# Kernel tuning notes

Measured on AMD Instinct MI355X. Metric: run time of the kernel, lower is better.

Reference implementation:

```python
import jax, jax.numpy as jnp
import numpy as np

H = 1024   # hidden_dim
I = 256    # input_dim
T = 128    # time_step
NW = 4     # input_num (weeks)
N = 100    # stocks = 5 categories * 20
C, G = 5, 20


def gru(x, Wih, Whh, bih, bhh):
    """Torch-style single-layer GRU. x: (B,T,I) batch_first -> (B,T,H). Gate order r,z,n."""
    gx = jnp.einsum('bti,gi->btg', x, Wih) + bih  # (B,T,3H) input projections precomputed
    h0 = jnp.zeros((x.shape[0], Whh.shape[1]), x.dtype)

    def step(h, g):
        gh = h @ Whh.T + bhh
        xr, xz, xn = jnp.split(g, 3, axis=-1)
        hr, hz, hn = jnp.split(gh, 3, axis=-1)
        r = jax.nn.sigmoid(xr + hr)
        z = jax.nn.sigmoid(xz + hz)
        n = jnp.tanh(xn + r * hn)
        h = (1.0 - z) * n + z * h
        return h, h

    _, ys = jax.lax.scan(step, h0, jnp.swapaxes(gx, 0, 1))
    return jnp.swapaxes(ys, 0, 1)


def att_block(x, W, b):
    """AttentionBlock: x (B,T,D); Linear over time axis, softmax over time, weighted sum."""
    xt = jnp.swapaxes(x, 1, 2)                    # (B,D,T)
    probs = jax.nn.softmax(xt @ W.T + b, axis=-1) # (B,D,T)
    probs = jnp.swapaxes(probs, 1, 2)             # (B,T,D)
    return (probs * x).sum(axis=1)                # (B,D)


def gat(x, edges, W, a_s, a_d, bias):
    """PyG GATConv, heads=1, add_self_loops=True, leaky_relu slope 0.2."""
    n = x.shape[0]
    h = x @ W.T                                   # (n,H)
    loop = jnp.arange(n)
    src = jnp.concatenate([edges[0], loop])
    dst = jnp.concatenate([edges[1], loop])
    e = jax.nn.leaky_relu((h @ a_s)[src] + (h @ a_d)[dst], 0.2)
    m = jax.ops.segment_max(e, dst, num_segments=n)
    ex = jnp.exp(e - m[dst])
    s = jax.ops.segment_sum(ex, dst, num_segments=n)
    alpha = ex / s[dst]
    return jax.ops.segment_sum(alpha[:, None] * h[src], dst, num_segments=n) + bias


def setup_inputs() -> dict:
    key = jax.random.key(0)
    ks = iter(jax.random.split(key, 64))
    p = lambda *s: jax.random.normal(next(ks), s, dtype=jnp.float32) * 0.05
    inp = {}
    for i in range(NW):
        inp[f'w{i}'] = jax.random.normal(next(ks), (N, T, I), dtype=jnp.float32)
    inp['inner_edge'] = jax.random.randint(next(ks), (2, 2000), 0, N, dtype=jnp.int32)
    inp['outer_edge'] = jax.random.randint(next(ks), (2, 25), 0, C, dtype=jnp.int32)
    # per-week sequence encoders (stacked)
    inp['enc_Wih'] = p(NW, 3 * H, I); inp['enc_Whh'] = p(NW, 3 * H, H)
    inp['enc_bih'] = p(NW, 3 * H);    inp['enc_bhh'] = p(NW, 3 * H)
    inp['enc_attW'] = p(NW, T, T);    inp['enc_attb'] = p(NW, T)
    # weekly GRU (not batch_first in torch!)
    inp['wk_Wih'] = p(3 * H, H); inp['wk_Whh'] = p(3 * H, H)
    inp['wk_bih'] = p(3 * H);    inp['wk_bhh'] = p(3 * H)
    inp['wkatt_W'] = p(NW, NW); inp['wkatt_b'] = p(NW)
    inp['pool_W'] = p(G, G);    inp['pool_b'] = p(G)
    inp['ig_W'] = p(H, H); inp['ig_as'] = p(H); inp['ig_ad'] = p(H); inp['ig_b'] = p(H)
    inp['cg_W'] = p(H, H); inp['cg_as'] = p(H); inp['cg_ad'] = p(H); inp['cg_b'] = p(H)
    inp['fus_W'] = p(H, 3 * H); inp['fus_b'] = p(H)
    inp['reg_W'] = p(1, H); inp['reg_b'] = p(1)
    inp['cls_W'] = p(1, H); inp['cls_b'] = p(1)
    return inp


def reference(w0, w1, w2, w3, inner_edge, outer_edge,
              enc_Wih, enc_Whh, enc_bih, enc_bhh, enc_attW, enc_attb,
              wk_Wih, wk_Whh, wk_bih, wk_bhh, wkatt_W, wkatt_b,
              pool_W, pool_b, ig_W, ig_as, ig_ad, ig_b,
              cg_W, cg_as, cg_ad, cg_b, fus_W, fus_b,
              reg_W, reg_b, cls_W, cls_b):
    weeks = [w0, w1, w2, w3]
    embs = []
    for i in range(NW):
        seq = gru(weeks[i], enc_Wih[i], enc_Whh[i], enc_bih[i], enc_bhh[i])  # (N,T,H)
        embs.append(att_block(seq, enc_attW[i], enc_attb[i])[:, None, :])    # (N,1,H)
    we = jnp.concatenate(embs, axis=1)                                       # (N,NW,H)
    # torch nn.GRU default seq-major: scans over dim0 (N stocks), batch=NW
    we = jnp.swapaxes(gru(jnp.swapaxes(we, 0, 1), wk_Wih, wk_Whh, wk_bih, wk_bhh), 0, 1)
    wav = att_block(we, wkatt_W, wkatt_b)                                    # (N,H)
    inner = gat(wav, inner_edge, ig_W, ig_as, ig_ad, ig_b).reshape(C, G, -1)
    wav3 = wav.reshape(C, G, -1)
    cat = att_block(wav3, pool_W, pool_b)                                    # (C,H)
    cat = gat(cat, outer_edge, cg_W, cg_as, cg_ad, cg_b)                     # (C,H)
    cat = jnp.broadcast_to(cat[:, None, :], (C, G, cat.shape[-1]))
    f = jnp.concatenate([wav3, cat, inner], axis=-1)                         # (C,G,3H)
    f = jax.nn.relu(f @ fus_W.T + fus_b)
    reg = (f @ reg_W.T + reg_b).reshape(-1)
    cls = jax.nn.sigmoid(f @ cls_W.T + cls_b).reshape(-1)
    return reg, cls
```

## Files before the change

kernel.cpp:

```cpp
#include <hip/hip_runtime.h>
#include <hip/hip_bf16.h>

#define NW 4
#define NST 100
#define TT 128
#define II 256
#define HH 1024
#define H3 3072

typedef _Float16 h8 __attribute__((ext_vector_type(8)));
typedef float f4 __attribute__((ext_vector_type(4)));

__device__ __forceinline__ float sigf(float x) { return 1.0f / (1.0f + expf(-x)); }

__device__ __forceinline__ float4 ld_f4_sc1(const float* p) {
    union { unsigned long long u[2]; float4 v; } r;
    r.u[0] = __hip_atomic_load((unsigned long long*)p, __ATOMIC_RELAXED, __HIP_MEMORY_SCOPE_AGENT);
    r.u[1] = __hip_atomic_load((unsigned long long*)p + 1, __ATOMIC_RELAXED, __HIP_MEMORY_SCOPE_AGENT);
    return r.v;
}
__device__ __forceinline__ float ld_f_sc1(const float* p) {
    return __hip_atomic_load((float*)p, __ATOMIC_RELAXED, __HIP_MEMORY_SCOPE_AGENT);
}

__device__ __forceinline__ void spin_wait(unsigned* f, unsigned t) {
    int guard = 0;
    while (__hip_atomic_load(f, __ATOMIC_RELAXED, __HIP_MEMORY_SCOPE_AGENT) <= t) {
        __builtin_amdgcn_s_sleep(1);
        if (++guard > (1 << 21)) break;
    }
}

__global__ void zero_k(float* a, int n) {
    int i = blockIdx.x * 256 + threadIdx.x;
    if (i < n) a[i] = 0.0f;
}

__global__ void convW_k(const float* __restrict__ Whh, const float* __restrict__ Wih,
                        _Float16* __restrict__ Wc) {
    int col = blockIdx.x * 256 + threadIdx.x;
    int r = blockIdx.y;
    int w = blockIdx.z;
    float v = (col < HH) ? Whh[((size_t)w * H3 + r) * HH + col]
                         : Wih[((size_t)w * H3 + r) * II + (col - HH)];
    Wc[((size_t)w * H3 + r) * 1280 + col] = (_Float16)v;
}

__global__ void convWk_k(const float* __restrict__ src, _Float16* __restrict__ dst) {
    int col = blockIdx.x * 256 + threadIdx.x;
    int r = blockIdx.y;
    dst[(size_t)r * HH + col] = (_Float16)src[(size_t)r * HH + col];
}

__global__ void xcvt_k(const float* __restrict__ x0, const float* __restrict__ x1,
                       const float* __restrict__ x2, const float* __restrict__ x3,
                       _Float16* __restrict__ xT) {
    int idx = blockIdx.x * 256 + threadIdx.x;
    int k8 = idx & 31;
    int m  = (idx >> 5) & 127;
    int t  = (idx >> 12) & 127;
    int w  = idx >> 19;
    const float* xw = (w == 0) ? x0 : (w == 1) ? x1 : (w == 2) ? x2 : x3;
    h8 hv = {};
    if (m < NST) {
        const float* s = xw + ((size_t)m * TT + t) * II + k8 * 8;
        float4 fa = *(const float4*)s;
        float4 fb = *(const float4*)(s + 4);
        hv[0] = (_Float16)fa.x; hv[1] = (_Float16)fa.y;
        hv[2] = (_Float16)fa.z; hv[3] = (_Float16)fa.w;
        hv[4] = (_Float16)fb.x; hv[5] = (_Float16)fb.y;
        hv[6] = (_Float16)fb.z; hv[7] = (_Float16)fb.w;
    }
    *(h8*)&xT[(((size_t)w * TT + t) * 128 + m) * II + k8 * 8] = hv;
}

__global__ void wTcvt_k(const float* __restrict__ attW, float* __restrict__ wT) {
    int tp = threadIdx.x;
    int t  = blockIdx.x;
    int w  = blockIdx.y;
    wT[((size_t)w * TT + t) * TT + tp] = attW[((size_t)w * TT + tp) * TT + t];
}

__global__ void convB_k(const float* __restrict__ bih, const float* __restrict__ bhh,
                        float* __restrict__ bc) {
    int j = blockIdx.x * 256 + threadIdx.x;
    int w = blockIdx.y;
    const float* bi = bih + w * H3;
    const float* bh = bhh + w * H3;
    float* o = bc + w * 4096;
    o[j] = bi[j] + bh[j];
    o[1024 + j] = bi[1024 + j] + bh[1024 + j];
    o[2048 + j] = bi[2048 + j];
    o[3072 + j] = bh[2048 + j];
}

#define ENC_LDS_HALFS (40 * 3 * 16 * 32)
#define ENC_LDS_BYTES (ENC_LDS_HALFS * 2)

__global__ __launch_bounds__(256) void enc_fused_k(
    const _Float16* __restrict__ Wc, const float* __restrict__ bc,
    const _Float16* __restrict__ xT,
    _Float16* __restrict__ hhA, _Float16* __restrict__ hhB,
    _Float16* __restrict__ seq, unsigned* flags)
{
    extern __shared__ _Float16 Bs[];

    int id = blockIdx.x;
    int rr = id & 7, qq = id >> 3;
    int w  = rr >> 1;
    int bx = qq * 2 + (rr & 1);
    int j0 = bx * 16;

    const _Float16* Wcw = Wc + (size_t)w * H3 * 1280;
    const float* bcw = bc + w * 4096;
    _Float16* hA = hhA + (size_t)w * 128 * HH;
    _Float16* hB = hhB + (size_t)w * 128 * HH;
    unsigned* fw = flags + (size_t)w * 64 * 16;

    int tid = threadIdx.x;
    int lane = tid & 63, wi = tid >> 6, quad = lane >> 4, l15 = lane & 15;

    if (tid < 192) {
        int brow = tid >> 2, bseg = tid & 3;
        int g = brow >> 4, jj = brow & 15;
        const _Float16* bsrc =
            Wcw + (size_t)(g * 1024 + j0 + jj) * 1280 + bseg * 8;
        #pragma unroll 8
        for (int c = 0; c < 40; c++) {
            uint4 v = *(const uint4*)(bsrc + c * 32);
            *(uint4*)&Bs[(((size_t)c * 3 + g) * 16 + jj) * 32 + bseg * 8] = v;
        }
    }
    __syncthreads();

    int j = j0 + l15;
    float br = bcw[j], bz = bcw[1024 + j], bni = bcw[2048 + j], bnh = bcw[3072 + j];
    int r0 = wi * 32 + l15, r1 = wi * 32 + 16 + l15;
    float hreg[2][4] = {};

    for (int t = 0; t < TT; t++) {
        const _Float16* hin = (t & 1) ? hB : hA;
        _Float16* hout = (t & 1) ? hA : hB;
        const _Float16* xt = xT + ((size_t)w * TT + t) * 128 * II;
        const _Float16* pA0h = hin + (size_t)r0 * HH + quad * 8;
        const _Float16* pA1h = hin + (size_t)r1 * HH + quad * 8;
        const _Float16* pA0x = xt + (size_t)r0 * II + quad * 8;
        const _Float16* pA1x = xt + (size_t)r1 * II + quad * 8;

        f4 aR[2] = {}, aZ[2] = {}, aNH[2] = {}, aNX[2] = {};

        h8 rb0[8], rb1[8];
        #pragma unroll
        for (int u = 0; u < 8; u++) {
            rb0[u] = *(const h8*)(pA0h + u * 32);
            rb1[u] = *(const h8*)(pA1h + u * 32);
        }

        #pragma unroll 8
        for (int c = 0; c < 40; c++) {
            int u = c & 7;
            h8 a0 = rb0[u], a1 = rb1[u];
            int cn = c + 8;
            if (cn < 32) {
                rb0[u] = *(const h8*)(pA0h + cn * 32);
                rb1[u] = *(const h8*)(pA1h + cn * 32);
            } else if (cn < 40) {
                rb0[u] = *(const h8*)(pA0x + (cn - 32) * 32);
                rb1[u] = *(const h8*)(pA1x + (cn - 32) * 32);
            }
            const _Float16* bb = &Bs[(size_t)c * 1536];
            h8 bf0 = *(const h8*)&bb[l15 * 32 + quad * 8];
            h8 bf1 = *(const h8*)&bb[512 + l15 * 32 + quad * 8];
            h8 bf2 = *(const h8*)&bb[1024 + l15 * 32 + quad * 8];
            aR[0] = __builtin_amdgcn_mfma_f32_16x16x32_f16(a0, bf0, aR[0], 0, 0, 0);
            aR[1] = __builtin_amdgcn_mfma_f32_16x16x32_f16(a1, bf0, aR[1], 0, 0, 0);
            aZ[0] = __builtin_amdgcn_mfma_f32_16x16x32_f16(a0, bf1, aZ[0], 0, 0, 0);
            aZ[1] = __builtin_amdgcn_mfma_f32_16x16x32_f16(a1, bf1, aZ[1], 0, 0, 0);
            if (c < 32) {
                aNH[0] = __builtin_amdgcn_mfma_f32_16x16x32_f16(a0, bf2, aNH[0], 0, 0, 0);
                aNH[1] = __builtin_amdgcn_mfma_f32_16x16x32_f16(a1, bf2, aNH[1], 0, 0, 0);
            } else {
                aNX[0] = __builtin_amdgcn_mfma_f32_16x16x32_f16(a0, bf2, aNX[0], 0, 0, 0);
                aNX[1] = __builtin_amdgcn_mfma_f32_16x16x32_f16(a1, bf2, aNX[1], 0, 0, 0);
            }
        }

        unsigned pks[2][4];
        #pragma unroll
        for (int mi = 0; mi < 2; mi++) {
            #pragma unroll
            for (int p = 0; p < 4; p++) {
                int row = wi * 32 + mi * 16 + quad * 4 + p;
                float r = sigf(aR[mi][p] + br);
                float z = sigf(aZ[mi][p] + bz);
                float n = tanhf(aNX[mi][p] + bni + r * (aNH[mi][p] + bnh));
                float hv = (1.f - z) * n + z * hreg[mi][p];
                hreg[mi][p] = hv;
                unsigned short hb = __builtin_bit_cast(unsigned short, (_Float16)hv);
                unsigned ob = __shfl_xor((unsigned)hb, 1);
                unsigned pk = (unsigned)hb | (ob << 16);
                pks[mi][p] = pk;
                if (!(l15 & 1) && t < TT - 1)
                    __hip_atomic_exchange((unsigned*)&hout[(size_t)row * HH + j], pk,
                                          __ATOMIC_RELAXED, __HIP_MEMORY_SCOPE_AGENT);
            }
        }
        if (t < TT - 1) {
            __syncthreads();
            if (tid == 0)
                __hip_atomic_store(&fw[bx * 16], (unsigned)(t + 1),
                                   __ATOMIC_RELAXED, __HIP_MEMORY_SCOPE_AGENT);
        }
        #pragma unroll
        for (int mi = 0; mi < 2; mi++) {
            #pragma unroll
            for (int p = 0; p < 4; p++) {
                int row = wi * 32 + mi * 16 + quad * 4 + p;
                if (!(l15 & 1) && row < NST)
                    __hip_atomic_store(
                        (unsigned*)&seq[(((size_t)w * NST + row) * TT + t) * HH + j],
                        pks[mi][p], __ATOMIC_RELAXED, __HIP_MEMORY_SCOPE_AGENT);
            }
        }
        if (t < TT - 1) {
            if (tid < 64) spin_wait(&fw[tid * 16], (unsigned)t);
            __syncthreads();
            __builtin_amdgcn_fence(__ATOMIC_ACQUIRE, "agent");
        }
    }
}

__global__ __launch_bounds__(256) void att1_k(
    const _Float16* __restrict__ seq, const float* __restrict__ wT,
    const float* __restrict__ attb, float* __restrict__ wex)
{
    int d0 = blockIdx.x * 128;
    int n  = blockIdx.y;
    int w  = blockIdx.z;
    __shared__ _Float16 S[128][128];
    __shared__ float PM[16][136];
    int tid = threadIdx.x;
    const _Float16* sp = seq + ((size_t)(w * NST + n) * TT) * HH + d0;
    for (int q = tid; q < 2048; q += 256) {
        int t = q >> 4, seg = q & 15;
        *(h8*)&S[t][seg * 8] = *(const h8*)(sp + (size_t)t * HH + seg * 8);
    }
    __syncthreads();
    int tx = tid & 15, ty = tid >> 4;
    const float* Wg = wT + (size_t)w * TT * TT;
    float acc[8][8];
    #pragma unroll
    for (int i = 0; i < 8; i++) {
        float b = attb[w * TT + ty * 8 + i];
        for (int j = 0; j < 8; j++) acc[i][j] = b;
    }
    for (int t = 0; t < 128; t++) {
        float wv[8], sv[8];
        float4 wa = *(const float4*)&Wg[(size_t)t * TT + ty * 8];
        float4 wb = *(const float4*)&Wg[(size_t)t * TT + ty * 8 + 4];
        wv[0] = wa.x; wv[1] = wa.y; wv[2] = wa.z; wv[3] = wa.w;
        wv[4] = wb.x; wv[5] = wb.y; wv[6] = wb.z; wv[7] = wb.w;
        h8 s8 = *(const h8*)&S[t][tx * 8];
        #pragma unroll
        for (int j = 0; j < 8; j++) sv[j] = (float)s8[j];
        #pragma unroll
        for (int i = 0; i < 8; i++)
            #pragma unroll
            for (int j = 0; j < 8; j++) acc[i][j] += wv[i] * sv[j];
    }
    float cmax[8], csum[8];
    #pragma unroll
    for (int j = 0; j < 8; j++) {
        float m = acc[0][j];
        for (int i = 1; i < 8; i++) m = fmaxf(m, acc[i][j]);
        PM[ty][tx * 8 + j] = m;
    }
    __syncthreads();
    #pragma unroll
    for (int j = 0; j < 8; j++) {
        float m = -1e30f;
        for (int yy = 0; yy < 16; yy++) m = fmaxf(m, PM[yy][tx * 8 + j]);
        cmax[j] = m;
    }
    __syncthreads();
    #pragma unroll
    for (int j = 0; j < 8; j++) {
        float s = 0.f;
        for (int i = 0; i < 8; i++) { acc[i][j] = expf(acc[i][j] - cmax[j]); s += acc[i][j]; }
        PM[ty][tx * 8 + j] = s;
    }
    __syncthreads();
    #pragma unroll
    for (int j = 0; j < 8; j++) {
        float s = 0.f;
        for (int yy = 0; yy < 16; yy++) s += PM[yy][tx * 8 + j];
        csum[j] = s;
    }
    __syncthreads();
    #pragma unroll
    for (int i = 0; i < 8; i++) {
        h8 s8 = *(const h8*)&S[ty * 8 + i][tx * 8];
        #pragma unroll
        for (int j = 0; j < 8; j++) {
            if (i == 0) PM[ty][tx * 8 + j] = 0.f;
            PM[ty][tx * 8 + j] += acc[i][j] * (float)s8[j];
        }
    }
    __syncthreads();
    if (ty == 0) {
        #pragma unroll
        for (int j = 0; j < 8; j++) {
            float o = 0.f;
            for (int yy = 0; yy < 16; yy++) o += PM[yy][tx * 8 + j];
            wex[((size_t)w * NST + n) * HH + d0 + tx * 8 + j] = o / csum[j];
        }
    }
}

template <int RELU>
__global__ __launch_bounds__(256) void gemm_tn_k(
    const float* __restrict__ A, const float* __restrict__ B,
    const float* __restrict__ bias, float* __restrict__ C, int M, int N, int K)
{
    int n0 = blockIdx.x * 64, m0 = blockIdx.y * 64;
    __shared__ float As[16][64], Bs[16][64];
    int tid = threadIdx.x, tx = tid & 15, ty = tid >> 4;
    float acc[4][4] = {{0.f}};
    for (int k0 = 0; k0 < K; k0 += 16) {
        __syncthreads();
        for (int q = tid; q < 1024; q += 256) {
            int kk = q & 15, r = q >> 4;
            int m = m0 + r, nn = n0 + r;
            As[kk][r] = (m < M) ? A[(size_t)m * K + k0 + kk] : 0.f;
            Bs[kk][r] = (nn < N) ? B[(size_t)nn * K + k0 + kk] : 0.f;
        }
        __syncthreads();
        #pragma unroll
        for (int kk = 0; kk < 16; kk++) {
            float4 av = *(const float4*)&As[kk][ty * 4];
            float4 bv = *(const float4*)&Bs[kk][tx * 4];
            float a[4] = {av.x, av.y, av.z, av.w};
            float b[4] = {bv.x, bv.y, bv.z, bv.w};
            #pragma unroll
            for (int r = 0; r < 4; r++)
                #pragma unroll
                for (int c = 0; c < 4; c++) acc[r][c] += a[r] * b[c];
        }
    }
    #pragma unroll
    for (int r = 0; r < 4; r++) {
        int m = m0 + ty * 4 + r;
        if (m >= M) continue;
        #pragma unroll
        for (int c = 0; c < 4; c++) {
            int nn = n0 + tx * 4 + c;
            if (nn >= N) continue;
            float v = acc[r][c] + (bias ? bias[nn] : 0.f);
            if (RELU) v = fmaxf(v, 0.f);
            C[(size_t)m * N + nn] = v;
        }
    }
}

__global__ __launch_bounds__(256) void wk_fused_k(
    const float* __restrict__ gxw, const _Float16* __restrict__ wkW,
    const float* __restrict__ bhh, float* __restrict__ hA,
    float* __restrict__ hB, float* __restrict__ we2, unsigned* flags)
{
    int tid = threadIdx.x;
    int wi = tid >> 6, lane = tid & 63;
    int j = blockIdx.x * 4 + wi;
    int k0 = lane * 16;
    float wf[3][16];
    #pragma unroll
    for (int g = 0; g < 3; g++) {
        h8 wa = *(const h8*)&wkW[(size_t)(g * HH + j) * HH + k0];
        h8 wb = *(const h8*)&wkW[(size_t)(g * HH + j) * HH + k0 + 8];
        #pragma unroll
        for (int i = 0; i < 8; i++) { wf[g][i] = (float)wa[i]; wf[g][8 + i] = (float)wb[i]; }
    }
    float b0 = bhh[j], b1 = bhh[HH + j], b2 = bhh[2 * HH + j];

    for (int t = 0; t < NST; t++) {
        const float* hin = (t & 1) ? hB : hA;
        float* hout = (t & 1) ? hA : hB;
        float acc[4][3] = {};
        #pragma unroll
        for (int b = 0; b < 4; b++) {
            float hv[16];
            #pragma unroll
            for (int s = 0; s < 4; s++) {
                float4 hq = ld_f4_sc1(&hin[b * HH + k0 + s * 4]);
                hv[s * 4] = hq.x; hv[s * 4 + 1] = hq.y;
                hv[s * 4 + 2] = hq.z; hv[s * 4 + 3] = hq.w;
            }
            #pragma unroll
            for (int g = 0; g < 3; g++)
                #pragma unroll
                for (int i = 0; i < 16; i++) acc[b][g] += wf[g][i] * hv[i];
        }
        #pragma unroll
        for (int b = 0; b < 4; b++)
            #pragma unroll
            for (int g = 0; g < 3; g++)
                for (int o = 32; o; o >>= 1) acc[b][g] += __shfl_down(acc[b][g], o);
        if (lane == 0) {
            for (int b = 0; b < 4; b++) {
                const float* gx = gxw + ((size_t)b * NST + t) * H3;
                float hr = acc[b][0] + b0;
                float hz = acc[b][1] + b1;
                float hn = acc[b][2] + b2;
                float r = sigf(gx[j] + hr);
                float z = sigf(gx[HH + j] + hz);
                float n = tanhf(gx[2 * HH + j] + r * hn);
                float hv = (1.f - z) * n + z * ld_f_sc1(&hin[b * HH + j]);
                __hip_atomic_exchange(&hout[b * HH + j], hv,
                                      __ATOMIC_RELAXED, __HIP_MEMORY_SCOPE_AGENT);
                we2[((size_t)t * 4 + b) * HH + j] = hv;
            }
        }
        if (t < NST - 1) {
            __syncthreads();
            if (tid == 0)
                __hip_atomic_store(&flags[blockIdx.x * 16], (unsigned)(t + 1),
                                   __ATOMIC_RELAXED, __HIP_MEMORY_SCOPE_AGENT);
            spin_wait(&flags[tid * 16], (unsigned)t);
            __syncthreads();
        }
    }
}

__global__ void wkatt_k(const float* __restrict__ we2, const float* __restrict__ W,
                        const float* __restrict__ bv, float* __restrict__ wav)
{
    int n = blockIdx.x;
    for (int d = threadIdx.x; d < HH; d += 256) {
        float v[4], l[4];
        #pragma unroll
        for (int tp = 0; tp < 4; tp++) v[tp] = we2[((size_t)n * 4 + tp) * HH + d];
        float mx = -1e30f;
        #pragma unroll
        for (int tp = 0; tp < 4; tp++) {
            float s = bv[tp];
            for (int t2 = 0; t2 < 4; t2++) s += v[t2] * W[tp * 4 + t2];
            l[tp] = s; mx = fmaxf(mx, s);
        }
        float se = 0.f, o = 0.f;
        #pragma unroll
        for (int tp = 0; tp < 4; tp++) {
            float e = expf(l[tp] - mx);
            se += e; o += e * v[tp];
        }
        wav[(size_t)n * HH + d] = o / se;
    }
}

__global__ void poolatt_k(const float* __restrict__ wav, const float* __restrict__ W,
                          const float* __restrict__ bv, float* __restrict__ cat1)
{
    int c = blockIdx.x;
    for (int d = threadIdx.x; d < HH; d += 256) {
        float v[20], l[20];
        for (int t2 = 0; t2 < 20; t2++) v[t2] = wav[((size_t)c * 20 + t2) * HH + d];
        float mx = -1e30f;
        for (int tp = 0; tp < 20; tp++) {
            float s = bv[tp];
            for (int t2 = 0; t2 < 20; t2++) s += v[t2] * W[tp * 20 + t2];
            l[tp] = s; mx = fmaxf(mx, s);
        }
        float se = 0.f, o = 0.f;
        for (int tp = 0; tp < 20; tp++) {
            float e = expf(l[tp] - mx);
            se += e; o += e * v[tp];
        }
        cat1[(size_t)c * HH + d] = o / se;
    }
}

__global__ void gat_dots_k(const float* __restrict__ h, const float* __restrict__ as_,
                           const float* __restrict__ ad_, float* __restrict__ ss,
                           float* __restrict__ sd)
{
    int i = blockIdx.x, tid = threadIdx.x;
    float s1 = 0.f, s2 = 0.f;
    for (int k = tid; k < HH; k += 256) {
        float v = h[(size_t)i * HH + k];
        s1 += v * as_[k]; s2 += v * ad_[k];
    }
    __shared__ float r1[256], r2[256];
    r1[tid] = s1; r2[tid] = s2; __syncthreads();
    for (int s = 128; s; s >>= 1) {
        if (tid < s) { r1[tid] += r1[tid + s]; r2[tid] += r2[tid + s]; }
        __syncthreads();
    }
    if (tid == 0) { ss[i] = r1[0]; sd[i] = r2[0]; }
}

#define MAXE 256
__global__ __launch_bounds__(256) void gat_agg_k(
    const float* __restrict__ hmat, const int* __restrict__ esrc,
    const int* __restrict__ edst, int nedges, const float* __restrict__ ss,
    const float* __restrict__ sd, const float* __restrict__ bias, float* __restrict__ outp)
{
    int i = blockIdx.x, tid = threadIdx.x;
    __shared__ int cnt;
    __shared__ int msrc[MAXE];
    __shared__ float mw[MAXE];
    __shared__ float inv_s;
    if (tid == 0) {
        cnt = 1; msrc[0] = i;
        float e = ss[i] + sd[i];
        mw[0] = e > 0.f ? e : 0.2f * e;
    }
    __syncthreads();
    for (int e = tid; e < nedges; e += 256) {
        if (edst[e] == i) {
            int p = atomicAdd(&cnt, 1);
            if (p < MAXE) {
                int s = esrc[e];
                msrc[p] = s;
                float v = ss[s] + sd[i];
                mw[p] = v > 0.f ? v : 0.2f * v;
            }
        }
    }
    __syncthreads();
    int m = min(cnt, MAXE);
    if (tid == 0) {
        float mx = -1e30f;
        for (int p = 0; p < m; p++) mx = fmaxf(mx, mw[p]);
        float s = 0.f;
        for (int p = 0; p < m; p++) { float e = expf(mw[p] - mx); mw[p] = e; s += e; }
        inv_s = 1.0f / s;
    }
    __syncthreads();
    for (int d = tid; d < HH; d += 256) {
        float a = 0.f;
        for (int p = 0; p < m; p++) a += mw[p] * hmat[(size_t)msrc[p] * HH + d];
        outp[(size_t)i * HH + d] = a * inv_s + bias[d];
    }
}

__global__ void concat_k(const float* __restrict__ wav, const float* __restrict__ gc,
                         const float* __restrict__ gi, float* __restrict__ cc)
{
    int row = blockIdx.x;
    int c = row / 20;
    for (int k = threadIdx.x; k < H3; k += 256) {
        float v;
        if (k < HH) v = wav[(size_t)row * HH + k];
        else if (k < 2 * HH) v = gc[(size_t)c * HH + (k - HH)];
        else v = gi[(size_t)row * HH + (k - 2 * HH)];
        cc[(size_t)row * H3 + k] = v;
    }
}

__global__ void heads_k(const float* __restrict__ f, const float* __restrict__ regW,
                        const float* __restrict__ regb, const float* __restrict__ clsW,
                        const float* __restrict__ clsb, float* __restrict__ outp)
{
    int i = blockIdx.x, tid = threadIdx.x;
    float s1 = 0.f, s2 = 0.f;
    for (int k = tid; k < HH; k += 256) {
        float v = f[(size_t)i * HH + k];
        s1 += v * regW[k]; s2 += v * clsW[k];
    }
    __shared__ float r1[256], r2[256];
    r1[tid] = s1; r2[tid] = s2; __syncthreads();
    for (int s = 128; s; s >>= 1) {
        if (tid < s) { r1[tid] += r1[tid + s]; r2[tid] += r2[tid + s]; }
        __syncthreads();
    }
    if (tid == 0) {
        outp[i] = r1[0] + regb[0];
        outp[100 + i] = sigf(r2[0] + clsb[0]);
    }
}

extern "C" void kernel_launch(void* const* d_in, const int* in_sizes, int n_in,
                              void* d_out, int out_size, void* d_ws, size_t ws_size,
                              hipStream_t stream)
{
    (void)in_sizes; (void)n_in; (void)out_size; (void)ws_size;
    const float* x0 = (const float*)d_in[0];
    const float* x1 = (const float*)d_in[1];
    const float* x2 = (const float*)d_in[2];
    const float* x3 = (const float*)d_in[3];
    const int*   ie = (const int*)d_in[4];
    const int*   oe = (const int*)d_in[5];
    const float* enc_Wih = (const float*)d_in[6];
    const float* enc_Whh = (const float*)d_in[7];
    const float* enc_bih = (const float*)d_in[8];
    const float* enc_bhh = (const float*)d_in[9];
    const float* enc_attW = (const float*)d_in[10];
    const float* enc_attb = (const float*)d_in[11];
    const float* wk_Wih = (const float*)d_in[12];
    const float* wk_Whh = (const float*)d_in[13];
    const float* wk_bih = (const float*)d_in[14];
    const float* wk_bhh = (const float*)d_in[15];
    const float* wkatt_W = (const float*)d_in[16];
    const float* wkatt_b = (const float*)d_in[17];
    const float* pool_W = (const float*)d_in[18];
    const float* pool_b = (const float*)d_in[19];
    const float* ig_W = (const float*)d_in[20];
    const float* ig_as = (const float*)d_in[21];
    const float* ig_ad = (const float*)d_in[22];
    const float* ig_b = (const float*)d_in[23];
    const float* cg_W = (const float*)d_in[24];
    const float* cg_as = (const float*)d_in[25];
    const float* cg_ad = (const float*)d_in[26];
    const float* cg_b = (const float*)d_in[27];
    const float* fus_W = (const float*)d_in[28];
    const float* fus_b = (const float*)d_in[29];
    const float* reg_W = (const float*)d_in[30];
    const float* reg_b = (const float*)d_in[31];
    const float* cls_W = (const float*)d_in[32];
    const float* cls_b = (const float*)d_in[33];
    float* outp = (float*)d_out;

    char* p = (char*)d_ws;
    auto alloc = [&](size_t bytes) { char* r = p; p += (bytes + 255) & ~(size_t)255; return (void*)r; };
    unsigned* flags = (unsigned*)alloc(2 * 256 * 16 * 4);
    _Float16* Wcat = (_Float16*)alloc((size_t)NW * H3 * 1280 * 2);
    float* bc = (float*)alloc((size_t)NW * 4 * HH * 4);
    _Float16* wkW = (_Float16*)alloc((size_t)H3 * HH * 2);
    _Float16* xT = (_Float16*)alloc((size_t)NW * TT * 128 * II * 2);
    float* wT = (float*)alloc((size_t)NW * TT * TT * 4);
    _Float16* hhA = (_Float16*)alloc((size_t)NW * 128 * HH * 2);
    _Float16* hhB = (_Float16*)alloc((size_t)NW * 128 * HH * 2);
    _Float16* seq = (_Float16*)alloc((size_t)NW * NST * TT * HH * 2);
    float* wex = (float*)alloc((size_t)NW * NST * HH * 4);
    float* gxw = (float*)alloc((size_t)NW * NST * H3 * 4);
    float* hwA = (float*)alloc(4 * HH * 4);
    float* hwB = (float*)alloc(4 * HH * 4);
    float* we2 = (float*)alloc((size_t)NST * 4 * HH * 4);
    float* wav = (float*)alloc((size_t)NST * HH * 4);
    float* hi  = (float*)alloc((size_t)NST * HH * 4);
    float* si_s = (float*)alloc(128 * 4);
    float* si_d = (float*)alloc(128 * 4);
    float* gi  = (float*)alloc((size_t)NST * HH * 4);
    float* cat1 = (float*)alloc(5 * HH * 4);
    float* hc  = (float*)alloc(5 * HH * 4);
    float* sc_s = (float*)alloc(64 * 4);
    float* sc_d = (float*)alloc(64 * 4);
    float* gc  = (float*)alloc(5 * HH * 4);
    float* cc  = (float*)alloc((size_t)NST * H3 * 4);
    float* fbuf = (float*)alloc((size_t)NST * HH * 4);

    static bool attr_done = false;
    if (!attr_done) {
        hipFuncSetAttribute((const void*)enc_fused_k,
                            hipFuncAttributeMaxDynamicSharedMemorySize, ENC_LDS_BYTES);
        attr_done = true;
    }

    zero_k<<<32, 256, 0, stream>>>((float*)flags, 2 * 256 * 16);
    convW_k<<<dim3(5, H3, NW), 256, 0, stream>>>(enc_Whh, enc_Wih, Wcat);
    convB_k<<<dim3(4, NW), 256, 0, stream>>>(enc_bih, enc_bhh, bc);
    convWk_k<<<dim3(4, H3), 256, 0, stream>>>(wk_Whh, wkW);
    xcvt_k<<<8192, 256, 0, stream>>>(x0, x1, x2, x3, xT);
    wTcvt_k<<<dim3(TT, NW), 128, 0, stream>>>(enc_attW, wT);
    zero_k<<<(NW * 128 * HH / 2 + 255) / 256, 256, 0, stream>>>((float*)hhA, NW * 128 * HH / 2);
    zero_k<<<(4 * HH + 255) / 256, 256, 0, stream>>>(hwA, 4 * HH);

    enc_fused_k<<<256, 256, ENC_LDS_BYTES, stream>>>(
        Wcat, bc, xT, hhA, hhB, seq, flags);

    att1_k<<<dim3(8, NST, NW), 256, 0, stream>>>(seq, wT, enc_attb, wex);

    gemm_tn_k<0><<<dim3(48, 7), 256, 0, stream>>>(wex, wk_Wih, wk_bih, gxw, 400, H3, HH);

    wk_fused_k<<<256, 256, 0, stream>>>(gxw, wkW, wk_bhh, hwA, hwB, we2, flags + 256 * 16);

    wkatt_k<<<NST, 256, 0, stream>>>(we2, wkatt_W, wkatt_b, wav);

    gemm_tn_k<0><<<dim3(16, 2), 256, 0, stream>>>(wav, ig_W, nullptr, hi, NST, HH, HH);
    gat_dots_k<<<NST, 256, 0, stream>>>(hi, ig_as, ig_ad, si_s, si_d);
    gat_agg_k<<<NST, 256, 0, stream>>>(hi, ie, ie + 2000, 2000, si_s, si_d, ig_b, gi);

    poolatt_k<<<5, 256, 0, stream>>>(wav, pool_W, pool_b, cat1);
    gemm_tn_k<0><<<dim3(16, 1), 256, 0, stream>>>(cat1, cg_W, nullptr, hc, 5, HH, HH);
    gat_dots_k<<<5, 256, 0, stream>>>(hc, cg_as, cg_ad, sc_s, sc_d);
    gat_agg_k<<<5, 256, 0, stream>>>(hc, oe, oe + 25, 25, sc_s, sc_d, cg_b, gc);

    concat_k<<<NST, 256, 0, stream>>>(wav, gc, gi, cc);
    gemm_tn_k<1><<<dim3(16, 2), 256, 0, stream>>>(cc, fus_W, fus_b, fbuf, NST, HH, H3);
    heads_k<<<NST, 256, 0, stream>>>(fbuf, reg_W, reg_b, cls_W, cls_b, outp);
}
```

Measured before the change: 5.142 ms.

## Use leader-block generation barrier, prefetch x into registers, fast transcendental math

```diff
diff --git a/kernel.cpp b/kernel.cpp
--- a/kernel.cpp
+++ b/kernel.cpp
@@ -11,7 +11,8 @@
 typedef _Float16 h8 __attribute__((ext_vector_type(8)));
 typedef float f4 __attribute__((ext_vector_type(4)));
 
-__device__ __forceinline__ float sigf(float x) { return 1.0f / (1.0f + expf(-x)); }
+__device__ __forceinline__ float sigf(float x) { return 1.0f / (1.0f + __expf(-x)); }
+__device__ __forceinline__ float tanhfast(float x) { return 1.0f - 2.0f / (1.0f + __expf(2.0f * x)); }
 
 __device__ __forceinline__ float4 ld_f4_sc1(const float* p) {
     union { unsigned long long u[2]; float4 v; } r;
@@ -27,7 +28,7 @@
     int guard = 0;
     while (__hip_atomic_load(f, __ATOMIC_RELAXED, __HIP_MEMORY_SCOPE_AGENT) <= t) {
         __builtin_amdgcn_s_sleep(1);
-        if (++guard > (1 << 21)) break;
+        if (++guard > (1 << 20)) break;
     }
 }
 
@@ -116,6 +117,7 @@
     _Float16* hA = hhA + (size_t)w * 128 * HH;
     _Float16* hB = hhB + (size_t)w * 128 * HH;
     unsigned* fw = flags + (size_t)w * 64 * 16;
+    unsigned* genw = flags + (size_t)(256 + w) * 16;
 
     int tid = threadIdx.x;
     int lane = tid & 63, wi = tid >> 6, quad = lane >> 4, l15 = lane & 15;
@@ -138,35 +140,44 @@
     int r0 = wi * 32 + l15, r1 = wi * 32 + 16 + l15;
     float hreg[2][4] = {};
 
+    h8 xb0[8], xb1[8];
+    {
+        const _Float16* x0p = xT + ((size_t)w * TT) * 128 * II;
+        #pragma unroll
+        for (int u = 0; u < 8; u++) {
+            xb0[u] = *(const h8*)(x0p + (size_t)r0 * II + quad * 8 + u * 32);
+            xb1[u] = *(const h8*)(x0p + (size_t)r1 * II + quad * 8 + u * 32);
+        }
+    }
+
     for (int t = 0; t < TT; t++) {
         const _Float16* hin = (t & 1) ? hB : hA;
         _Float16* hout = (t & 1) ? hA : hB;
-        const _Float16* xt = xT + ((size_t)w * TT + t) * 128 * II;
         const _Float16* pA0h = hin + (size_t)r0 * HH + quad * 8;
         const _Float16* pA1h = hin + (size_t)r1 * HH + quad * 8;
-        const _Float16* pA0x = xt + (size_t)r0 * II + quad * 8;
-        const _Float16* pA1x = xt + (size_t)r1 * II + quad * 8;
 
         f4 aR[2] = {}, aZ[2] = {}, aNH[2] = {}, aNX[2] = {};
 
-        h8 rb0[8], rb1[8];
-        #pragma unroll
-        for (int u = 0; u < 8; u++) {
+        h8 rb0[12], rb1[12];
+        #pragma unroll
+        for (int u = 0; u < 12; u++) {
             rb0[u] = *(const h8*)(pA0h + u * 32);
             rb1[u] = *(const h8*)(pA1h + u * 32);
         }
 
-        #pragma unroll 8
+        #pragma unroll
         for (int c = 0; c < 40; c++) {
-            int u = c & 7;
-            h8 a0 = rb0[u], a1 = rb1[u];
-            int cn = c + 8;
-            if (cn < 32) {
-                rb0[u] = *(const h8*)(pA0h + cn * 32);
-                rb1[u] = *(const h8*)(pA1h + cn * 32);
-            } else if (cn < 40) {
-                rb0[u] = *(const h8*)(pA0x + (cn - 32) * 32);
-                rb1[u] = *(const h8*)(pA1x + (cn - 32) * 32);
+            h8 a0, a1;
+            if (c < 32) {
+                int u = c % 12;
+                a0 = rb0[u]; a1 = rb1[u];
+                int cn = c + 12;
+                if (cn < 32) {
+                    rb0[u] = *(const h8*)(pA0h + cn * 32);
+                    rb1[u] = *(const h8*)(pA1h + cn * 32);
+                }
+            } else {
+                a0 = xb0[c - 32]; a1 = xb1[c - 32];
             }
             const _Float16* bb = &Bs[(size_t)c * 1536];
             h8 bf0 = *(const h8*)&bb[l15 * 32 + quad * 8];
@@ -193,7 +204,7 @@
                 int row = wi * 32 + mi * 16 + quad * 4 + p;
                 float r = sigf(aR[mi][p] + br);
                 float z = sigf(aZ[mi][p] + bz);
-                float n = tanhf(aNX[mi][p] + bni + r * (aNH[mi][p] + bnh));
+                float n = tanhfast(aNX[mi][p] + bni + r * (aNH[mi][p] + bnh));
                 float hv = (1.f - z) * n + z * hreg[mi][p];
                 hreg[mi][p] = hv;
                 unsigned short hb = __builtin_bit_cast(unsigned short, (_Float16)hv);
@@ -223,8 +234,22 @@
             }
         }
         if (t < TT - 1) {
-            if (tid < 64) spin_wait(&fw[tid * 16], (unsigned)t);
-            __syncthreads();
+            const _Float16* xn = xT + ((size_t)w * TT + t + 1) * 128 * II;
+            #pragma unroll
+            for (int u = 0; u < 8; u++) {
+                xb0[u] = *(const h8*)(xn + (size_t)r0 * II + quad * 8 + u * 32);
+                xb1[u] = *(const h8*)(xn + (size_t)r1 * II + quad * 8 + u * 32);
+            }
+            if (bx == 0) {
+                if (tid < 64) spin_wait(&fw[tid * 16], (unsigned)t);
+                __syncthreads();
+                if (tid == 0)
+                    __hip_atomic_store(genw, (unsigned)(t + 1),
+                                       __ATOMIC_RELAXED, __HIP_MEMORY_SCOPE_AGENT);
+            } else {
+                if (tid == 0) spin_wait(genw, (unsigned)t);
+                __syncthreads();
+            }
             __builtin_amdgcn_fence(__ATOMIC_ACQUIRE, "agent");
         }
     }
@@ -371,6 +396,7 @@
     int wi = tid >> 6, lane = tid & 63;
     int j = blockIdx.x * 4 + wi;
     int k0 = lane * 16;
+    unsigned* gen = flags + 256 * 16;
     float wf[3][16];
     #pragma unroll
     for (int g = 0; g < 3; g++) {
@@ -412,7 +438,7 @@
                 float hn = acc[b][2] + b2;
                 float r = sigf(gx[j] + hr);
                 float z = sigf(gx[HH + j] + hz);
-                float n = tanhf(gx[2 * HH + j] + r * hn);
+                float n = tanhfast(gx[2 * HH + j] + r * hn);
                 float hv = (1.f - z) * n + z * ld_f_sc1(&hin[b * HH + j]);
                 __hip_atomic_exchange(&hout[b * HH + j], hv,
                                       __ATOMIC_RELAXED, __HIP_MEMORY_SCOPE_AGENT);
@@ -424,8 +450,16 @@
             if (tid == 0)
                 __hip_atomic_store(&flags[blockIdx.x * 16], (unsigned)(t + 1),
                                    __ATOMIC_RELAXED, __HIP_MEMORY_SCOPE_AGENT);
-            spin_wait(&flags[tid * 16], (unsigned)t);
-            __syncthreads();
+            if (blockIdx.x == 0) {
+                spin_wait(&flags[tid * 16], (unsigned)t);
+                __syncthreads();
+                if (tid == 0)
+                    __hip_atomic_store(gen, (unsigned)(t + 1),
+                                       __ATOMIC_RELAXED, __HIP_MEMORY_SCOPE_AGENT);
+            } else {
+                if (tid == 0) spin_wait(gen, (unsigned)t);
+                __syncthreads();
+            }
         }
     }
 }
@@ -620,7 +654,7 @@
 
     char* p = (char*)d_ws;
     auto alloc = [&](size_t bytes) { char* r = p; p += (bytes + 255) & ~(size_t)255; return (void*)r; };
-    unsigned* flags = (unsigned*)alloc(2 * 256 * 16 * 4);
+    unsigned* flags = (unsigned*)alloc(1024 * 16 * 4);
     _Float16* Wcat = (_Float16*)alloc((size_t)NW * H3 * 1280 * 2);
     float* bc = (float*)alloc((size_t)NW * 4 * HH * 4);
     _Float16* wkW = (_Float16*)alloc((size_t)H3 * HH * 2);
@@ -654,7 +688,7 @@
         attr_done = true;
     }
 
-    zero_k<<<32, 256, 0, stream>>>((float*)flags, 2 * 256 * 16);
+    zero_k<<<64, 256, 0, stream>>>((float*)flags, 1024 * 16);
     convW_k<<<dim3(5, H3, NW), 256, 0, stream>>>(enc_Whh, enc_Wih, Wcat);
     convB_k<<<dim3(4, NW), 256, 0, stream>>>(enc_bih, enc_bhh, bc);
     convWk_k<<<dim3(4, H3), 256, 0, stream>>>(wk_Whh, wkW);
@@ -670,7 +704,7 @@
 
     gemm_tn_k<0><<<dim3(48, 7), 256, 0, stream>>>(wex, wk_Wih, wk_bih, gxw, 400, H3, HH);
 
-    wk_fused_k<<<256, 256, 0, stream>>>(gxw, wkW, wk_bhh, hwA, hwB, we2, flags + 256 * 16);
+    wk_fused_k<<<256, 256, 0, stream>>>(gxw, wkW, wk_bhh, hwA, hwB, we2, flags + 512 * 16);
 
     wkatt_k<<<NST, 256, 0, stream>>>(we2, wkatt_W, wkatt_b, wav);
 
```

After: 4.599 ms. -10.6%, faster.
